# Performance work log

Hardware: AMD Instinct MI355X
Metric: run time of the kernel (lower is better)

The kernel has to match this reference:

```python
import jax, jax.numpy as jnp
import numpy as np

B, T, I, H = 64, 2048, 256, 256


def setup_inputs() -> dict:
    key = jax.random.key(0)
    ks = jax.random.split(key, 9)
    s = 1.0 / np.sqrt(H).astype(np.float32)  # torch nn.RNN init: U(-1/sqrt(H), 1/sqrt(H))
    u = lambda k, shape: jax.random.uniform(k, shape, jnp.float32, -s, s)
    return {
        "input_feature": jax.random.normal(ks[0], (B, T, I), jnp.float32),
        "W_ih0": u(ks[1], (H, I)),
        "W_hh0": u(ks[2], (H, H)),
        "b_ih0": u(ks[3], (H,)),
        "b_hh0": u(ks[4], (H,)),
        "W_ih1": u(ks[5], (H, H)),
        "W_hh1": u(ks[6], (H, H)),
        "b_ih1": u(ks[7], (H,)),
        "b_hh1": u(ks[8], (H,)),
    }


def _rnn_layer(x, W_ih, W_hh, b_ih, b_hh):
    # x: [B, T, F]. Precompute the input projection for all timesteps at once,
    # then scan the recurrence: h_t = tanh(x_t W_ih^T + b_ih + h_{t-1} W_hh^T + b_hh)
    pre = jnp.einsum("btf,hf->bth", x, W_ih) + b_ih + b_hh  # [B, T, H]
    h0 = jnp.zeros((x.shape[0], W_hh.shape[0]), x.dtype)

    def step(h, p):
        h_new = jnp.tanh(p + h @ W_hh.T)
        return h_new, h_new

    _, ys = jax.lax.scan(step, h0, jnp.swapaxes(pre, 0, 1))  # [T, B, H]
    return jnp.swapaxes(ys, 0, 1)  # [B, T, H]


def reference(input_feature, W_ih0, W_hh0, b_ih0, b_hh0, W_ih1, W_hh1, b_ih1, b_hh1):
    # hidden_0 = zeros, batch_first=True, tanh nonlinearity (torch.nn.RNN default)
    h = _rnn_layer(input_feature, W_ih0, W_hh0, b_ih0, b_hh0)
    h = _rnn_layer(h, W_ih1, W_hh1, b_ih1, b_hh1)
    return h  # output: [B, T, H] (module returns only `output`)
```

## Files before the change

kernel.cpp:

```cpp
#include <hip/hip_runtime.h>
#include <stdint.h>

#define B_ 64
#define T_ 2048
#define H_ 256
#define S_ 64
#define C_ (T_ / S_)

typedef unsigned int u32;
typedef unsigned short u16;
typedef __attribute__((ext_vector_type(8))) short short8;
typedef __attribute__((ext_vector_type(4))) float f32x4;

#define SWZ(row, byte) (((row) * 512) + ((byte) ^ (((row) & 7) << 4)))

static __device__ __forceinline__ u32 cvtpk(float a, float b) {
  u32 d;
  asm("v_cvt_pk_bf16_f32 %0, %1, %2" : "=v"(d) : "v"(a), "v"(b));
  return d;
}
static __device__ __forceinline__ uint4 pack8(float4 a, float4 b) {
  uint4 r;
  r.x = cvtpk(a.x, a.y); r.y = cvtpk(a.z, a.w);
  r.z = cvtpk(b.x, b.y); r.w = cvtpk(b.z, b.w);
  return r;
}
static __device__ __forceinline__ short8 as8(uint4 v) {
  return __builtin_bit_cast(short8, v);
}
static __device__ __forceinline__ f32x4 mfma4(uint4 a, uint4 b, f32x4 c) {
  return __builtin_amdgcn_mfma_f32_16x16x32_bf16(as8(a), as8(b), c, 0, 0, 0);
}
static __device__ __forceinline__ float fast_tanh(float x) {
  float e = __expf(2.0f * x);
  float r = __builtin_amdgcn_rcpf(e + 1.0f);
  return fmaf(-2.0f, r, 1.0f);
}

template <int NQ>
static __device__ __forceinline__ void load_wfrag(const float* W, int qbase, int bl,
                                                  int g, uint4 wf[NQ][8]) {
#pragma unroll
  for (int q = 0; q < NQ; ++q) {
    const float* wr = W + (size_t)((qbase + q) * 16 + bl) * H_ + g * 8;
#pragma unroll
    for (int kc = 0; kc < 8; ++kc) {
      float4 a = *(const float4*)(wr + kc * 32);
      float4 b = *(const float4*)(wr + kc * 32 + 4);
      wf[q][kc] = pack8(a, b);
    }
  }
}

static __device__ void proj0_body(char* smem, const float* X, const float* Wih0,
                                  const float* bih0, const float* bhh0,
                                  float* dout, int ch, int bid2) {
  const int tid = threadIdx.x;
  const int lane = tid & 63, wv = tid >> 6;
  const int bl = lane & 15, g = lane >> 4;
  char* sb0 = smem;
  char* sb1 = smem + 8192;

  uint4 wf[2][8];
  load_wfrag<2>(Wih0, wv * 2, bl, g, wf);
  float4 cb[2];
#pragma unroll
  for (int q = 0; q < 2; ++q) {
    const int j0 = (wv * 2 + q) * 16 + g * 4;
    float4 a = *(const float4*)(bih0 + j0);
    float4 b = *(const float4*)(bhh0 + j0);
    cb[q].x = a.x + b.x; cb[q].y = a.y + b.y;
    cb[q].z = a.z + b.z; cb[q].w = a.w + b.w;
  }

  const int sr = tid >> 5, sc8 = (tid & 31) * 8;
  auto rowbase = [&](int it) -> size_t {
    const int b = bid2 * 2 + (it >> 2), i = it & 3;
    return (size_t)(b * T_ + ch * S_ + i * 16);
  };
  float4 s0, s1;
  {
    const float4* xs = (const float4*)(X + (rowbase(0) + sr) * H_ + sc8);
    s0 = xs[0]; s1 = xs[1];
  }

  for (int it = 0; it < 8; ++it) {
    char* sb = (it & 1) ? sb1 : sb0;
    *(uint4*)(sb + SWZ(sr, sc8 * 2)) = pack8(s0, s1);
    __syncthreads();
    if (it + 1 < 8) {
      const float4* xn = (const float4*)(X + (rowbase(it + 1) + sr) * H_ + sc8);
      s0 = xn[0]; s1 = xn[1];
    }
    uint4 hf[8];
#pragma unroll
    for (int kc = 0; kc < 8; ++kc)
      hf[kc] = *(const uint4*)(sb + SWZ(bl, kc * 64 + g * 16));
    f32x4 acc[2];
#pragma unroll
    for (int q = 0; q < 2; ++q) {
      acc[q] = (f32x4){0.f, 0.f, 0.f, 0.f};
#pragma unroll
      for (int kc = 0; kc < 8; ++kc)
        acc[q] = mfma4(wf[q][kc], hf[kc], acc[q]);
    }
    float* od = dout + (rowbase(it) + bl) * H_;
#pragma unroll
    for (int q = 0; q < 2; ++q) {
      const int j0 = (wv * 2 + q) * 16 + g * 4;
      float4 o;
      o.x = acc[q][0] + cb[q].x; o.y = acc[q][1] + cb[q].y;
      o.z = acc[q][2] + cb[q].z; o.w = acc[q][3] + cb[q].w;
      *(float4*)(od + j0) = o;
    }
    __syncthreads();
  }
}

__global__ __launch_bounds__(512, 1) void pre_chunk0(const float* X, const float* Wih0,
                                                     const float* bih0, const float* bhh0,
                                                     float* dout) {
  __shared__ __align__(16) char smem[2 * 8192];
  proj0_body(smem, X, Wih0, bih0, bhh0, dout, 0, blockIdx.x);
}

__global__ __launch_bounds__(256, 2) void pre_mfma(const float* X, const float* W,
                                                   const float* bi, const float* bh,
                                                   float* P, int tpw) {
  __shared__ char sb_[2][8192];
  const int tid = threadIdx.x;
  const int lane = tid & 63, wv = tid >> 6;
  const int bl = lane & 15, g = lane >> 4;

  uint4 wf[4][8];
  load_wfrag<4>(W, wv * 4, bl, g, wf);
  float4 bias[4];
#pragma unroll
  for (int q = 0; q < 4; ++q) {
    const int j0 = (wv * 4 + q) * 16 + g * 4;
    float4 a = *(const float4*)(bi + j0);
    float4 c = *(const float4*)(bh + j0);
    bias[q].x = a.x + c.x; bias[q].y = a.y + c.y;
    bias[q].z = a.z + c.z; bias[q].w = a.w + c.w;
  }

  const size_t row0 = (size_t)blockIdx.x * tpw * 16;
  const int sr = tid >> 4, sc = (tid & 15) * 16;
  float4 s0, s1, s2, s3;
  {
    const float4* xs = (const float4*)(X + (row0 + sr) * H_ + sc);
    s0 = xs[0]; s1 = xs[1]; s2 = xs[2]; s3 = xs[3];
  }

  for (int i = 0; i < tpw; ++i) {
    char* sb = sb_[i & 1];
    *(uint4*)(sb + SWZ(sr, sc * 2)) = pack8(s0, s1);
    *(uint4*)(sb + SWZ(sr, sc * 2 + 16)) = pack8(s2, s3);
    __syncthreads();
    if (i + 1 < tpw) {
      const float4* xn = (const float4*)(X + (row0 + (i + 1) * 16 + sr) * H_ + sc);
      s0 = xn[0]; s1 = xn[1]; s2 = xn[2]; s3 = xn[3];
    }
    uint4 hf[8];
#pragma unroll
    for (int kc = 0; kc < 8; ++kc)
      hf[kc] = *(const uint4*)(sb + SWZ(bl, kc * 64 + g * 16));
    f32x4 acc[4];
#pragma unroll
    for (int q = 0; q < 4; ++q) {
      acc[q] = (f32x4){0.f, 0.f, 0.f, 0.f};
#pragma unroll
      for (int kc = 0; kc < 8; ++kc)
        acc[q] = mfma4(wf[q][kc], hf[kc], acc[q]);
    }
#pragma unroll
    for (int q = 0; q < 4; ++q) {
      const int j0 = (wv * 4 + q) * 16 + g * 4;
      float4 o;
      o.x = acc[q][0] + bias[q].x; o.y = acc[q][1] + bias[q].y;
      o.z = acc[q][2] + bias[q].z; o.w = acc[q][3] + bias[q].w;
      *(float4*)(P + (row0 + i * 16 + bl) * H_ + j0) = o;
    }
    __syncthreads();
  }
}

__global__ __launch_bounds__(512, 1) void rec_mfma(const float* pre, const float* W,
                                                   float* out) {
  __shared__ char hb_[2][8192];
  const int tid = threadIdx.x;
  const int lane = tid & 63, wv = tid >> 6;
  const int bl = lane & 15, g = lane >> 4;
  const int b0 = blockIdx.x * 16;

  uint4 wf[2][8];
  load_wfrag<2>(W, wv * 2, bl, g, wf);
  {
    uint4 z = make_uint4(0, 0, 0, 0);
    ((uint4*)hb_[0])[tid] = z;
    ((uint4*)hb_[1])[tid] = z;
  }
  const float* prow = pre + (size_t)(b0 + bl) * T_ * H_;
  float* orow = out + (size_t)(b0 + bl) * T_ * H_;
  float4 pr0[2], pr1[2];
#pragma unroll
  for (int q = 0; q < 2; ++q) {
    const int j0 = (wv * 2 + q) * 16 + g * 4;
    pr0[q] = *(const float4*)(prow + 0 * H_ + j0);
    pr1[q] = *(const float4*)(prow + 1 * H_ + j0);
  }
  __syncthreads();

  auto step = [&](int t, float4 (&pr)[2], char* rbuf, char* wbuf) {
    uint4 hf[8];
#pragma unroll
    for (int kc = 0; kc < 8; ++kc)
      hf[kc] = *(const uint4*)(rbuf + SWZ(bl, kc * 64 + g * 16));
    f32x4 accA[2], accB[2];
#pragma unroll
    for (int q = 0; q < 2; ++q) {
      accA[q] = (f32x4){0.f, 0.f, 0.f, 0.f};
      accB[q] = (f32x4){0.f, 0.f, 0.f, 0.f};
#pragma unroll
      for (int kc = 0; kc < 4; ++kc) {
        accA[q] = mfma4(wf[q][kc], hf[kc], accA[q]);
        accB[q] = mfma4(wf[q][kc + 4], hf[kc + 4], accB[q]);
      }
    }
#pragma unroll
    for (int q = 0; q < 2; ++q) {
      const int j0 = (wv * 2 + q) * 16 + g * 4;
      const float* pq = (const float*)&pr[q];
      float v0 = fast_tanh(accA[q][0] + accB[q][0] + pq[0]);
      float v1 = fast_tanh(accA[q][1] + accB[q][1] + pq[1]);
      float v2 = fast_tanh(accA[q][2] + accB[q][2] + pq[2]);
      float v3 = fast_tanh(accA[q][3] + accB[q][3] + pq[3]);
      uint2 hw; hw.x = cvtpk(v0, v1); hw.y = cvtpk(v2, v3);
      *(uint2*)(wbuf + SWZ(bl, j0 * 2)) = hw;
      float4 o; o.x = v0; o.y = v1; o.z = v2; o.w = v3;
      *(float4*)(orow + (size_t)t * H_ + j0) = o;
      if (t + 2 < T_)
        pr[q] = *(const float4*)(prow + (size_t)(t + 2) * H_ + j0);
    }
    asm volatile("s_waitcnt lgkmcnt(0)" ::: "memory");
    __builtin_amdgcn_s_barrier();
    __builtin_amdgcn_sched_barrier(0);
  };

  for (int t = 0; t < T_; t += 2) {
    step(t, pr0, hb_[0], hb_[1]);
    step(t + 1, pr1, hb_[1], hb_[0]);
  }
}

__global__ __launch_bounds__(512, 1) void chunk4_k(
    const float* X, float* dout, const float* Wih0, const float* bih0,
    const float* bhh0, const float* Whh0, const float* Wih1, const float* Whh1,
    const float* bih1, const float* bhh1,
    u16* ring, u16* carry0, u16* carry1, int c) {
  __shared__ __align__(16) char smem[2 * 8192];
  const int tid = threadIdx.x;
  const int lane = tid & 63, wv = tid >> 6;
  const int bl = lane & 15, g = lane >> 4;
  const int bid = blockIdx.x;
  char* sb0 = smem;
  char* sb1 = smem + 8192;

  if (bid < 4) {
    if (c >= C_) return;
    const int pair = bid;
    uint4 wf[2][8];
    load_wfrag<2>(Whh0, wv * 2, bl, g, wf);
    if (c == 0) {
      uint4 z = make_uint4(0, 0, 0, 0);
      ((uint4*)sb0)[tid] = z;
    } else {
      const u16* cr = carry0 + pair * 16 * H_ + bl * H_;
#pragma unroll
      for (int q = 0; q < 2; ++q) {
        const int j0 = (wv * 2 + q) * 16 + g * 4;
        uint2 hw = *(const uint2*)(cr + j0);
        *(uint2*)(sb0 + SWZ(bl, j0 * 2)) = hw;
      }
    }
    const float* prow = dout + (size_t)(pair * 16 + bl) * T_ * H_ + (size_t)c * S_ * H_;
    u16* rch = ring + ((size_t)(c & 1) * S_) * (B_ * H_) + (size_t)(pair * 16 + bl) * H_;
    float4 pr0[2], pr1[2];
#pragma unroll
    for (int q = 0; q < 2; ++q) {
      const int j0 = (wv * 2 + q) * 16 + g * 4;
      pr0[q] = *(const float4*)(prow + 0 * H_ + j0);
      pr1[q] = *(const float4*)(prow + 1 * H_ + j0);
    }
    __syncthreads();

    auto step = [&](int s, float4 (&pr)[2], char* rbuf, char* wbuf) {
      uint4 hf[8];
#pragma unroll
      for (int kc = 0; kc < 8; ++kc)
        hf[kc] = *(const uint4*)(rbuf + SWZ(bl, kc * 64 + g * 16));
      f32x4 accA[2], accB[2];
#pragma unroll
      for (int q = 0; q < 2; ++q) {
        accA[q] = (f32x4){0.f, 0.f, 0.f, 0.f};
        accB[q] = (f32x4){0.f, 0.f, 0.f, 0.f};
#pragma unroll
        for (int kc = 0; kc < 4; ++kc) {
          accA[q] = mfma4(wf[q][kc], hf[kc], accA[q]);
          accB[q] = mfma4(wf[q][kc + 4], hf[kc + 4], accB[q]);
        }
      }
#pragma unroll
      for (int q = 0; q < 2; ++q) {
        const int j0 = (wv * 2 + q) * 16 + g * 4;
        const float* pq = (const float*)&pr[q];
        float v0 = fast_tanh(accA[q][0] + accB[q][0] + pq[0]);
        float v1 = fast_tanh(accA[q][1] + accB[q][1] + pq[1]);
        float v2 = fast_tanh(accA[q][2] + accB[q][2] + pq[2]);
        float v3 = fast_tanh(accA[q][3] + accB[q][3] + pq[3]);
        uint2 hw; hw.x = cvtpk(v0, v1); hw.y = cvtpk(v2, v3);
        *(uint2*)(wbuf + SWZ(bl, j0 * 2)) = hw;
        *(uint2*)(rch + (size_t)s * (B_ * H_) + j0) = hw;
        if (s + 2 < S_)
          pr[q] = *(const float4*)(prow + (size_t)(s + 2) * H_ + j0);
      }
      asm volatile("s_waitcnt lgkmcnt(0)" ::: "memory");
      __builtin_amdgcn_s_barrier();
      __builtin_amdgcn_sched_barrier(0);
    };
    for (int s = 0; s < S_; s += 2) {
      step(s, pr0, sb0, sb1);
      step(s + 1, pr1, sb1, sb0);
    }
    {
      u16* cw = carry0 + pair * 16 * H_ + bl * H_;
#pragma unroll
      for (int q = 0; q < 2; ++q) {
        const int j0 = (wv * 2 + q) * 16 + g * 4;
        uint2 hw = *(const uint2*)(sb0 + SWZ(bl, j0 * 2));
        *(uint2*)(cw + j0) = hw;
      }
    }
  } else if (bid < 8) {
    if (c < 1 || c > C_) return;
    const int pair = bid - 4;
    const int ch = c - 1;
    uint4 wf[2][8];
    load_wfrag<2>(Wih1, wv * 2, bl, g, wf);
    float4 cb[2];
#pragma unroll
    for (int q = 0; q < 2; ++q) {
      const int j0 = (wv * 2 + q) * 16 + g * 4;
      float4 a = *(const float4*)(bih1 + j0);
      float4 b = *(const float4*)(bhh1 + j0);
      cb[q].x = a.x + b.x; cb[q].y = a.y + b.y;
      cb[q].z = a.z + b.z; cb[q].w = a.w + b.w;
    }
    const u16* rbase2 = ring + ((size_t)(ch & 1) * S_) * (B_ * H_) + (size_t)pair * 16 * H_;
    const int sr = tid >> 5, scb = (tid & 31) * 16;
    uint4 v = *(const uint4*)(rbase2 + 0 * (B_ * H_) + (size_t)sr * H_ + (tid & 31) * 8);

    for (int s = 0; s < S_; ++s) {
      char* sb = (s & 1) ? sb1 : sb0;
      *(uint4*)(sb + SWZ(sr, scb)) = v;
      __syncthreads();
      if (s + 1 < S_)
        v = *(const uint4*)(rbase2 + (size_t)(s + 1) * (B_ * H_) + (size_t)sr * H_ + (tid & 31) * 8);
      uint4 hf[8];
#pragma unroll
      for (int kc = 0; kc < 8; ++kc)
        hf[kc] = *(const uint4*)(sb + SWZ(bl, kc * 64 + g * 16));
      f32x4 acc[2];
#pragma unroll
      for (int q = 0; q < 2; ++q) {
        acc[q] = (f32x4){0.f, 0.f, 0.f, 0.f};
#pragma unroll
        for (int kc = 0; kc < 8; ++kc)
          acc[q] = mfma4(wf[q][kc], hf[kc], acc[q]);
      }
      float* od = dout + (size_t)(pair * 16 + bl) * T_ * H_ + (size_t)(ch * S_ + s) * H_;
#pragma unroll
      for (int q = 0; q < 2; ++q) {
        const int j0 = (wv * 2 + q) * 16 + g * 4;
        float4 o;
        o.x = acc[q][0] + cb[q].x; o.y = acc[q][1] + cb[q].y;
        o.z = acc[q][2] + cb[q].z; o.w = acc[q][3] + cb[q].w;
        *(float4*)(od + j0) = o;
      }
      __syncthreads();
    }
  } else if (bid < 12) {
    if (c < 2) return;
    const int pair = bid - 8;
    const int ch = c - 2;
    uint4 wf[2][8];
    load_wfrag<2>(Whh1, wv * 2, bl, g, wf);
    if (ch == 0) {
      uint4 z = make_uint4(0, 0, 0, 0);
      ((uint4*)sb0)[tid] = z;
    } else {
      const u16* cr = carry1 + pair * 16 * H_ + bl * H_;
#pragma unroll
      for (int q = 0; q < 2; ++q) {
        const int j0 = (wv * 2 + q) * 16 + g * 4;
        uint2 hw = *(const uint2*)(cr + j0);
        *(uint2*)(sb0 + SWZ(bl, j0 * 2)) = hw;
      }
    }
    float* prow = dout + (size_t)(pair * 16 + bl) * T_ * H_ + (size_t)ch * S_ * H_;
    float4 pr0[2], pr1[2];
#pragma unroll
    for (int q = 0; q < 2; ++q) {
      const int j0 = (wv * 2 + q) * 16 + g * 4;
      pr0[q] = *(const float4*)(prow + 0 * H_ + j0);
      pr1[q] = *(const float4*)(prow + 1 * H_ + j0);
    }
    __syncthreads();

    auto step = [&](int s, float4 (&pr)[2], char* rbuf, char* wbuf) {
      uint4 hf[8];
#pragma unroll
      for (int kc = 0; kc < 8; ++kc)
        hf[kc] = *(const uint4*)(rbuf + SWZ(bl, kc * 64 + g * 16));
      f32x4 accA[2], accB[2];
#pragma unroll
      for (int q = 0; q < 2; ++q) {
        accA[q] = (f32x4){0.f, 0.f, 0.f, 0.f};
        accB[q] = (f32x4){0.f, 0.f, 0.f, 0.f};
#pragma unroll
        for (int kc = 0; kc < 4; ++kc) {
          accA[q] = mfma4(wf[q][kc], hf[kc], accA[q]);
          accB[q] = mfma4(wf[q][kc + 4], hf[kc + 4], accB[q]);
        }
      }
#pragma unroll
      for (int q = 0; q < 2; ++q) {
        const int j0 = (wv * 2 + q) * 16 + g * 4;
        const float* pq = (const float*)&pr[q];
        float v0 = fast_tanh(accA[q][0] + accB[q][0] + pq[0]);
        float v1 = fast_tanh(accA[q][1] + accB[q][1] + pq[1]);
        float v2 = fast_tanh(accA[q][2] + accB[q][2] + pq[2]);
        float v3 = fast_tanh(accA[q][3] + accB[q][3] + pq[3]);
        uint2 hw; hw.x = cvtpk(v0, v1); hw.y = cvtpk(v2, v3);
        *(uint2*)(wbuf + SWZ(bl, j0 * 2)) = hw;
        float4 o; o.x = v0; o.y = v1; o.z = v2; o.w = v3;
        *(float4*)(prow + (size_t)s * H_ + j0) = o;
        if (s + 2 < S_)
          pr[q] = *(const float4*)(prow + (size_t)(s + 2) * H_ + j0);
      }
      asm volatile("s_waitcnt lgkmcnt(0)" ::: "memory");
      __builtin_amdgcn_s_barrier();
      __builtin_amdgcn_sched_barrier(0);
    };
    for (int s = 0; s < S_; s += 2) {
      step(s, pr0, sb0, sb1);
      step(s + 1, pr1, sb1, sb0);
    }
    {
      u16* cw = carry1 + pair * 16 * H_ + bl * H_;
#pragma unroll
      for (int q = 0; q < 2; ++q) {
        const int j0 = (wv * 2 + q) * 16 + g * 4;
        uint2 hw = *(const uint2*)(sb0 + SWZ(bl, j0 * 2));
        *(uint2*)(cw + j0) = hw;
      }
    }
  } else {
    if (c + 1 > C_ - 1) return;
    proj0_body(smem, X, Wih0, bih0, bhh0, dout, c + 1, bid - 12);
  }
}

extern "C" void kernel_launch(void* const* d_in, const int* in_sizes, int n_in,
                              void* d_out, int out_size, void* d_ws, size_t ws_size,
                              hipStream_t stream) {
  (void)in_sizes; (void)n_in; (void)out_size;
  const float* x    = (const float*)d_in[0];
  const float* Wih0 = (const float*)d_in[1];
  const float* Whh0 = (const float*)d_in[2];
  const float* bih0 = (const float*)d_in[3];
  const float* bhh0 = (const float*)d_in[4];
  const float* Wih1 = (const float*)d_in[5];
  const float* Whh1 = (const float*)d_in[6];
  const float* bih1 = (const float*)d_in[7];
  const float* bhh1 = (const float*)d_in[8];
  float* out = (float*)d_out;

  const size_t ring_elems = (size_t)2 * S_ * B_ * H_;
  const size_t carry_elems = (size_t)B_ * H_;
  const size_t need = (ring_elems + 2 * carry_elems) * sizeof(u16);

  if (ws_size >= need) {
    u16* ring = (u16*)d_ws;
    u16* carry0 = ring + ring_elems;
    u16* carry1 = carry0 + carry_elems;
    pre_chunk0<<<dim3(32), dim3(512), 0, stream>>>(x, Wih0, bih0, bhh0, out);
    for (int c = 0; c <= C_ + 1; ++c)
      chunk4_k<<<dim3(44), dim3(512), 0, stream>>>(
          x, out, Wih0, bih0, bhh0, Whh0, Wih1, Whh1, bih1, bhh1,
          ring, carry0, carry1, c);
  } else {
    const int TPW = 8;
    const int NWG = (B_ * T_) / (TPW * 16);
    pre_mfma<<<dim3(NWG), dim3(256), 0, stream>>>(x, Wih0, bih0, bhh0, out, TPW);
    rec_mfma<<<dim3(B_ / 16), dim3(512), 0, stream>>>(out, Whh0, out);
    pre_mfma<<<dim3(NWG), dim3(256), 0, stream>>>(out, Wih1, bih1, bhh1, out, TPW);
    rec_mfma<<<dim3(B_ / 16), dim3(512), 0, stream>>>(out, Whh1, out);
  }
}
```

Before: 2.431 ms.

## Replace per-chunk kernel launches with one persistent kernel using flag-based sync

```diff
diff --git a/kernel.cpp b/kernel.cpp
--- a/kernel.cpp
+++ b/kernel.cpp
@@ -52,26 +52,37 @@
   }
 }
 
+static __device__ __forceinline__ void wait_ge(u32* f, u32 tgt) {
+  if (__hip_atomic_load(f, __ATOMIC_ACQUIRE, __HIP_MEMORY_SCOPE_AGENT) >= tgt) return;
+  while (__hip_atomic_load(f, __ATOMIC_ACQUIRE, __HIP_MEMORY_SCOPE_AGENT) < tgt)
+    __builtin_amdgcn_s_sleep(8);
+}
+static __device__ __forceinline__ void drain_all() {
+  asm volatile("s_waitcnt vmcnt(0) lgkmcnt(0)" ::: "memory");
+  __builtin_amdgcn_s_barrier();
+}
+static __device__ __forceinline__ void publish_val(u32* f, u32 v) {
+  drain_all();
+  if (threadIdx.x == 0)
+    __hip_atomic_store(f, v, __ATOMIC_RELEASE, __HIP_MEMORY_SCOPE_AGENT);
+}
+static __device__ __forceinline__ void publish_add(u32* f) {
+  drain_all();
+  if (threadIdx.x == 0)
+    (void)__hip_atomic_fetch_add(f, 1u, __ATOMIC_RELEASE, __HIP_MEMORY_SCOPE_AGENT);
+}
+
+__global__ void init_flags(u32* f) { f[threadIdx.x] = 0; }
+
 static __device__ void proj0_body(char* smem, const float* X, const float* Wih0,
                                   const float* bih0, const float* bhh0,
-                                  float* dout, int ch, int bid2) {
+                                  float* dout, int ch, int bid2,
+                                  const uint4 wf[2][8], const float4 cb[2]) {
   const int tid = threadIdx.x;
   const int lane = tid & 63, wv = tid >> 6;
   const int bl = lane & 15, g = lane >> 4;
   char* sb0 = smem;
   char* sb1 = smem + 8192;
-
-  uint4 wf[2][8];
-  load_wfrag<2>(Wih0, wv * 2, bl, g, wf);
-  float4 cb[2];
-#pragma unroll
-  for (int q = 0; q < 2; ++q) {
-    const int j0 = (wv * 2 + q) * 16 + g * 4;
-    float4 a = *(const float4*)(bih0 + j0);
-    float4 b = *(const float4*)(bhh0 + j0);
-    cb[q].x = a.x + b.x; cb[q].y = a.y + b.y;
-    cb[q].z = a.z + b.z; cb[q].w = a.w + b.w;
-  }
 
   const int sr = tid >> 5, sc8 = (tid & 31) * 8;
   auto rowbase = [&](int it) -> size_t {
@@ -83,7 +94,6 @@
     const float4* xs = (const float4*)(X + (rowbase(0) + sr) * H_ + sc8);
     s0 = xs[0]; s1 = xs[1];
   }
-
   for (int it = 0; it < 8; ++it) {
     char* sb = (it & 1) ? sb1 : sb0;
     *(uint4*)(sb + SWZ(sr, sc8 * 2)) = pack8(s0, s1);
@@ -115,13 +125,6 @@
     }
     __syncthreads();
   }
-}
-
-__global__ __launch_bounds__(512, 1) void pre_chunk0(const float* X, const float* Wih0,
-                                                     const float* bih0, const float* bhh0,
-                                                     float* dout) {
-  __shared__ __align__(16) char smem[2 * 8192];
-  proj0_body(smem, X, Wih0, bih0, bhh0, dout, 0, blockIdx.x);
 }
 
 __global__ __launch_bounds__(256, 2) void pre_mfma(const float* X, const float* W,
@@ -143,7 +146,6 @@
     bias[q].x = a.x + c.x; bias[q].y = a.y + c.y;
     bias[q].z = a.z + c.z; bias[q].w = a.w + c.w;
   }
-
   const size_t row0 = (size_t)blockIdx.x * tpw * 16;
   const int sr = tid >> 4, sc = (tid & 15) * 16;
   float4 s0, s1, s2, s3;
@@ -151,7 +153,6 @@
     const float4* xs = (const float4*)(X + (row0 + sr) * H_ + sc);
     s0 = xs[0]; s1 = xs[1]; s2 = xs[2]; s3 = xs[3];
   }
-
   for (int i = 0; i < tpw; ++i) {
     char* sb = sb_[i & 1];
     *(uint4*)(sb + SWZ(sr, sc * 2)) = pack8(s0, s1);
@@ -246,18 +247,17 @@
     __builtin_amdgcn_s_barrier();
     __builtin_amdgcn_sched_barrier(0);
   };
-
   for (int t = 0; t < T_; t += 2) {
     step(t, pr0, hb_[0], hb_[1]);
     step(t + 1, pr1, hb_[1], hb_[0]);
   }
 }
 
-__global__ __launch_bounds__(512, 1) void chunk4_k(
-    const float* X, float* dout, const float* Wih0, const float* bih0,
-    const float* bhh0, const float* Whh0, const float* Wih1, const float* Whh1,
-    const float* bih1, const float* bhh1,
-    u16* ring, u16* carry0, u16* carry1, int c) {
+__global__ __launch_bounds__(512, 1) void persist_k(
+    const float* X, float* dout,
+    const float* Wih0, const float* bih0, const float* bhh0, const float* Whh0,
+    const float* Wih1, const float* Whh1, const float* bih1, const float* bhh1,
+    u16* ring, u32* flags) {
   __shared__ __align__(16) char smem[2 * 8192];
   const int tid = threadIdx.x;
   const int lane = tid & 63, wv = tid >> 6;
@@ -265,86 +265,74 @@
   const int bid = blockIdx.x;
   char* sb0 = smem;
   char* sb1 = smem + 8192;
+  u32* proj0_cnt = flags;
+  auto rec0_prog = [&](int p) { return flags + 32 + 32 * p; };
+  auto proj1_prog = [&](int p) { return flags + 160 + 32 * p; };
 
   if (bid < 4) {
-    if (c >= C_) return;
-    const int pair = bid;
+    const int p = bid;
     uint4 wf[2][8];
     load_wfrag<2>(Whh0, wv * 2, bl, g, wf);
-    if (c == 0) {
-      uint4 z = make_uint4(0, 0, 0, 0);
-      ((uint4*)sb0)[tid] = z;
-    } else {
-      const u16* cr = carry0 + pair * 16 * H_ + bl * H_;
+    { uint4 z = make_uint4(0, 0, 0, 0); ((uint4*)sb0)[tid] = z; }
+    __syncthreads();
+    const float* prow = dout + (size_t)(p * 16 + bl) * T_ * H_;
+    u16* rb = ring + (size_t)(p * 16 + bl) * H_;
+
+    for (int c = 0; c < C_; ++c) {
+      const u32 ptgt = 32u * (u32)((c + 2 < C_) ? (c + 2) : C_);
+      wait_ge(proj0_cnt, ptgt);
+      if (c >= 1) wait_ge(proj1_prog(p), (u32)(c - 1));
+      const float* pch = prow + (size_t)c * S_ * H_;
+      u16* rch = rb + ((size_t)(c & 1) * S_) * (B_ * H_);
+      float4 pr0[2], pr1[2];
 #pragma unroll
       for (int q = 0; q < 2; ++q) {
         const int j0 = (wv * 2 + q) * 16 + g * 4;
-        uint2 hw = *(const uint2*)(cr + j0);
-        *(uint2*)(sb0 + SWZ(bl, j0 * 2)) = hw;
-      }
-    }
-    const float* prow = dout + (size_t)(pair * 16 + bl) * T_ * H_ + (size_t)c * S_ * H_;
-    u16* rch = ring + ((size_t)(c & 1) * S_) * (B_ * H_) + (size_t)(pair * 16 + bl) * H_;
-    float4 pr0[2], pr1[2];
-#pragma unroll
-    for (int q = 0; q < 2; ++q) {
-      const int j0 = (wv * 2 + q) * 16 + g * 4;
-      pr0[q] = *(const float4*)(prow + 0 * H_ + j0);
-      pr1[q] = *(const float4*)(prow + 1 * H_ + j0);
-    }
-    __syncthreads();
-
-    auto step = [&](int s, float4 (&pr)[2], char* rbuf, char* wbuf) {
-      uint4 hf[8];
-#pragma unroll
-      for (int kc = 0; kc < 8; ++kc)
-        hf[kc] = *(const uint4*)(rbuf + SWZ(bl, kc * 64 + g * 16));
-      f32x4 accA[2], accB[2];
-#pragma unroll
-      for (int q = 0; q < 2; ++q) {
-        accA[q] = (f32x4){0.f, 0.f, 0.f, 0.f};
-        accB[q] = (f32x4){0.f, 0.f, 0.f, 0.f};
-#pragma unroll
-        for (int kc = 0; kc < 4; ++kc) {
-          accA[q] = mfma4(wf[q][kc], hf[kc], accA[q]);
-          accB[q] = mfma4(wf[q][kc + 4], hf[kc + 4], accB[q]);
-        }
-      }
-#pragma unroll
-      for (int q = 0; q < 2; ++q) {
-        const int j0 = (wv * 2 + q) * 16 + g * 4;
-        const float* pq = (const float*)&pr[q];
-        float v0 = fast_tanh(accA[q][0] + accB[q][0] + pq[0]);
-        float v1 = fast_tanh(accA[q][1] + accB[q][1] + pq[1]);
-        float v2 = fast_tanh(accA[q][2] + accB[q][2] + pq[2]);
-        float v3 = fast_tanh(accA[q][3] + accB[q][3] + pq[3]);
-        uint2 hw; hw.x = cvtpk(v0, v1); hw.y = cvtpk(v2, v3);
-        *(uint2*)(wbuf + SWZ(bl, j0 * 2)) = hw;
-        *(uint2*)(rch + (size_t)s * (B_ * H_) + j0) = hw;
-        if (s + 2 < S_)
-          pr[q] = *(const float4*)(prow + (size_t)(s + 2) * H_ + j0);
-      }
-      asm volatile("s_waitcnt lgkmcnt(0)" ::: "memory");
-      __builtin_amdgcn_s_barrier();
-      __builtin_amdgcn_sched_barrier(0);
-    };
-    for (int s = 0; s < S_; s += 2) {
-      step(s, pr0, sb0, sb1);
-      step(s + 1, pr1, sb1, sb0);
-    }
-    {
-      u16* cw = carry0 + pair * 16 * H_ + bl * H_;
-#pragma unroll
-      for (int q = 0; q < 2; ++q) {
-        const int j0 = (wv * 2 + q) * 16 + g * 4;
-        uint2 hw = *(const uint2*)(sb0 + SWZ(bl, j0 * 2));
-        *(uint2*)(cw + j0) = hw;
-      }
+        pr0[q] = *(const float4*)(pch + 0 * H_ + j0);
+        pr1[q] = *(const float4*)(pch + 1 * H_ + j0);
+      }
+      auto step = [&](int s, float4 (&pr)[2], char* rbuf, char* wbuf) {
+        uint4 hf[8];
+#pragma unroll
+        for (int kc = 0; kc < 8; ++kc)
+          hf[kc] = *(const uint4*)(rbuf + SWZ(bl, kc * 64 + g * 16));
+        f32x4 accA[2], accB[2];
+#pragma unroll
+        for (int q = 0; q < 2; ++q) {
+          accA[q] = (f32x4){0.f, 0.f, 0.f, 0.f};
+          accB[q] = (f32x4){0.f, 0.f, 0.f, 0.f};
+#pragma unroll
+          for (int kc = 0; kc < 4; ++kc) {
+            accA[q] = mfma4(wf[q][kc], hf[kc], accA[q]);
+            accB[q] = mfma4(wf[q][kc + 4], hf[kc + 4], accB[q]);
+          }
+        }
+#pragma unroll
+        for (int q = 0; q < 2; ++q) {
+          const int j0 = (wv * 2 + q) * 16 + g * 4;
+          const float* pq = (const float*)&pr[q];
+          float v0 = fast_tanh(accA[q][0] + accB[q][0] + pq[0]);
+          float v1 = fast_tanh(accA[q][1] + accB[q][1] + pq[1]);
+          float v2 = fast_tanh(accA[q][2] + accB[q][2] + pq[2]);
+          float v3 = fast_tanh(accA[q][3] + accB[q][3] + pq[3]);
+          uint2 hw; hw.x = cvtpk(v0, v1); hw.y = cvtpk(v2, v3);
+          *(uint2*)(wbuf + SWZ(bl, j0 * 2)) = hw;
+          *(uint2*)(rch + (size_t)s * (B_ * H_) + j0) = hw;
+          if (s + 2 < S_)
+            pr[q] = *(const float4*)(pch + (size_t)(s + 2) * H_ + j0);
+        }
+        asm volatile("s_waitcnt lgkmcnt(0)" ::: "memory");
+        __builtin_amdgcn_s_barrier();
+        __builtin_amdgcn_sched_barrier(0);
+      };
+      for (int s = 0; s < S_; s += 2) {
+        step(s, pr0, sb0, sb1);
+        step(s + 1, pr1, sb1, sb0);
+      }
+      publish_val(rec0_prog(p), (u32)(c + 1));
     }
   } else if (bid < 8) {
-    if (c < 1 || c > C_) return;
-    const int pair = bid - 4;
-    const int ch = c - 1;
+    const int p = bid - 4;
     uint4 wf[2][8];
     load_wfrag<2>(Wih1, wv * 2, bl, g, wf);
     float4 cb[2];
@@ -356,118 +344,117 @@
       cb[q].x = a.x + b.x; cb[q].y = a.y + b.y;
       cb[q].z = a.z + b.z; cb[q].w = a.w + b.w;
     }
-    const u16* rbase2 = ring + ((size_t)(ch & 1) * S_) * (B_ * H_) + (size_t)pair * 16 * H_;
     const int sr = tid >> 5, scb = (tid & 31) * 16;
-    uint4 v = *(const uint4*)(rbase2 + 0 * (B_ * H_) + (size_t)sr * H_ + (tid & 31) * 8);
-
-    for (int s = 0; s < S_; ++s) {
-      char* sb = (s & 1) ? sb1 : sb0;
-      *(uint4*)(sb + SWZ(sr, scb)) = v;
-      __syncthreads();
-      if (s + 1 < S_)
-        v = *(const uint4*)(rbase2 + (size_t)(s + 1) * (B_ * H_) + (size_t)sr * H_ + (tid & 31) * 8);
-      uint4 hf[8];
-#pragma unroll
-      for (int kc = 0; kc < 8; ++kc)
-        hf[kc] = *(const uint4*)(sb + SWZ(bl, kc * 64 + g * 16));
-      f32x4 acc[2];
-#pragma unroll
-      for (int q = 0; q < 2; ++q) {
-        acc[q] = (f32x4){0.f, 0.f, 0.f, 0.f};
+    for (int ch = 0; ch < C_; ++ch) {
+      wait_ge(rec0_prog(p), (u32)(ch + 1));
+      const u16* rbase2 = ring + ((size_t)(ch & 1) * S_) * (B_ * H_) + (size_t)p * 16 * H_;
+      uint4 v = *(const uint4*)(rbase2 + (size_t)sr * H_ + (tid & 31) * 8);
+      for (int s = 0; s < S_; ++s) {
+        char* sb = (s & 1) ? sb1 : sb0;
+        *(uint4*)(sb + SWZ(sr, scb)) = v;
+        __syncthreads();
+        if (s + 1 < S_)
+          v = *(const uint4*)(rbase2 + (size_t)(s + 1) * (B_ * H_) + (size_t)sr * H_ + (tid & 31) * 8);
+        uint4 hf[8];
 #pragma unroll
         for (int kc = 0; kc < 8; ++kc)
-          acc[q] = mfma4(wf[q][kc], hf[kc], acc[q]);
-      }
-      float* od = dout + (size_t)(pair * 16 + bl) * T_ * H_ + (size_t)(ch * S_ + s) * H_;
+          hf[kc] = *(const uint4*)(sb + SWZ(bl, kc * 64 + g * 16));
+        f32x4 acc[2];
+#pragma unroll
+        for (int q = 0; q < 2; ++q) {
+          acc[q] = (f32x4){0.f, 0.f, 0.f, 0.f};
+#pragma unroll
+          for (int kc = 0; kc < 8; ++kc)
+            acc[q] = mfma4(wf[q][kc], hf[kc], acc[q]);
+        }
+        float* od = dout + (size_t)(p * 16 + bl) * T_ * H_ + (size_t)(ch * S_ + s) * H_;
+#pragma unroll
+        for (int q = 0; q < 2; ++q) {
+          const int j0 = (wv * 2 + q) * 16 + g * 4;
+          float4 o;
+          o.x = acc[q][0] + cb[q].x; o.y = acc[q][1] + cb[q].y;
+          o.z = acc[q][2] + cb[q].z; o.w = acc[q][3] + cb[q].w;
+          *(float4*)(od + j0) = o;
+        }
+        __syncthreads();
+      }
+      publish_val(proj1_prog(p), (u32)(ch + 1));
+    }
+  } else if (bid < 12) {
+    const int p = bid - 8;
+    uint4 wf[2][8];
+    load_wfrag<2>(Whh1, wv * 2, bl, g, wf);
+    { uint4 z = make_uint4(0, 0, 0, 0); ((uint4*)sb0)[tid] = z; }
+    __syncthreads();
+    float* prow = dout + (size_t)(p * 16 + bl) * T_ * H_;
+
+    for (int ch = 0; ch < C_; ++ch) {
+      wait_ge(proj1_prog(p), (u32)(ch + 1));
+      float* pch = prow + (size_t)ch * S_ * H_;
+      float4 pr0[2], pr1[2];
 #pragma unroll
       for (int q = 0; q < 2; ++q) {
         const int j0 = (wv * 2 + q) * 16 + g * 4;
-        float4 o;
-        o.x = acc[q][0] + cb[q].x; o.y = acc[q][1] + cb[q].y;
-        o.z = acc[q][2] + cb[q].z; o.w = acc[q][3] + cb[q].w;
-        *(float4*)(od + j0) = o;
-      }
-      __syncthreads();
-    }
-  } else if (bid < 12) {
-    if (c < 2) return;
-    const int pair = bid - 8;
-    const int ch = c - 2;
+        pr0[q] = *(const float4*)(pch + 0 * H_ + j0);
+        pr1[q] = *(const float4*)(pch + 1 * H_ + j0);
+      }
+      auto step = [&](int s, float4 (&pr)[2], char* rbuf, char* wbuf) {
+        uint4 hf[8];
+#pragma unroll
+        for (int kc = 0; kc < 8; ++kc)
+          hf[kc] = *(const uint4*)(rbuf + SWZ(bl, kc * 64 + g * 16));
+        f32x4 accA[2], accB[2];
+#pragma unroll
+        for (int q = 0; q < 2; ++q) {
+          accA[q] = (f32x4){0.f, 0.f, 0.f, 0.f};
+          accB[q] = (f32x4){0.f, 0.f, 0.f, 0.f};
+#pragma unroll
+          for (int kc = 0; kc < 4; ++kc) {
+            accA[q] = mfma4(wf[q][kc], hf[kc], accA[q]);
+            accB[q] = mfma4(wf[q][kc + 4], hf[kc + 4], accB[q]);
+          }
+        }
+#pragma unroll
+        for (int q = 0; q < 2; ++q) {
+          const int j0 = (wv * 2 + q) * 16 + g * 4;
+          const float* pq = (const float*)&pr[q];
+          float v0 = fast_tanh(accA[q][0] + accB[q][0] + pq[0]);
+          float v1 = fast_tanh(accA[q][1] + accB[q][1] + pq[1]);
+          float v2 = fast_tanh(accA[q][2] + accB[q][2] + pq[2]);
+          float v3 = fast_tanh(accA[q][3] + accB[q][3] + pq[3]);
+          uint2 hw; hw.x = cvtpk(v0, v1); hw.y = cvtpk(v2, v3);
+          *(uint2*)(wbuf + SWZ(bl, j0 * 2)) = hw;
+          float4 o; o.x = v0; o.y = v1; o.z = v2; o.w = v3;
+          *(float4*)(pch + (size_t)s * H_ + j0) = o;
+          if (s + 2 < S_)
+            pr[q] = *(const float4*)(pch + (size_t)(s + 2) * H_ + j0);
+        }
+        asm volatile("s_waitcnt lgkmcnt(0)" ::: "memory");
+        __builtin_amdgcn_s_barrier();
+        __builtin_amdgcn_sched_barrier(0);
+      };
+      for (int s = 0; s < S_; s += 2) {
+        step(s, pr0, sb0, sb1);
+        step(s + 1, pr1, sb1, sb0);
+      }
+    }
+  } else {
+    const int b2 = bid - 12;
     uint4 wf[2][8];
-    load_wfrag<2>(Whh1, wv * 2, bl, g, wf);
-    if (ch == 0) {
-      uint4 z = make_uint4(0, 0, 0, 0);
-      ((uint4*)sb0)[tid] = z;
-    } else {
-      const u16* cr = carry1 + pair * 16 * H_ + bl * H_;
-#pragma unroll
-      for (int q = 0; q < 2; ++q) {
-        const int j0 = (wv * 2 + q) * 16 + g * 4;
-        uint2 hw = *(const uint2*)(cr + j0);
-        *(uint2*)(sb0 + SWZ(bl, j0 * 2)) = hw;
-      }
-    }
-    float* prow = dout + (size_t)(pair * 16 + bl) * T_ * H_ + (size_t)ch * S_ * H_;
-    float4 pr0[2], pr1[2];
+    load_wfrag<2>(Wih0, wv * 2, bl, g, wf);
+    float4 cb[2];
 #pragma unroll
     for (int q = 0; q < 2; ++q) {
       const int j0 = (wv * 2 + q) * 16 + g * 4;
-      pr0[q] = *(const float4*)(prow + 0 * H_ + j0);
-      pr1[q] = *(const float4*)(prow + 1 * H_ + j0);
-    }
-    __syncthreads();
-
-    auto step = [&](int s, float4 (&pr)[2], char* rbuf, char* wbuf) {
-      uint4 hf[8];
-#pragma unroll
-      for (int kc = 0; kc < 8; ++kc)
-        hf[kc] = *(const uint4*)(rbuf + SWZ(bl, kc * 64 + g * 16));
-      f32x4 accA[2], accB[2];
-#pragma unroll
-      for (int q = 0; q < 2; ++q) {
-        accA[q] = (f32x4){0.f, 0.f, 0.f, 0.f};
-        accB[q] = (f32x4){0.f, 0.f, 0.f, 0.f};
-#pragma unroll
-        for (int kc = 0; kc < 4; ++kc) {
-          accA[q] = mfma4(wf[q][kc], hf[kc], accA[q]);
-          accB[q] = mfma4(wf[q][kc + 4], hf[kc + 4], accB[q]);
-        }
-      }
-#pragma unroll
-      for (int q = 0; q < 2; ++q) {
-        const int j0 = (wv * 2 + q) * 16 + g * 4;
-        const float* pq = (const float*)&pr[q];
-        float v0 = fast_tanh(accA[q][0] + accB[q][0] + pq[0]);
-        float v1 = fast_tanh(accA[q][1] + accB[q][1] + pq[1]);
-        float v2 = fast_tanh(accA[q][2] + accB[q][2] + pq[2]);
-        float v3 = fast_tanh(accA[q][3] + accB[q][3] + pq[3]);
-        uint2 hw; hw.x = cvtpk(v0, v1); hw.y = cvtpk(v2, v3);
-        *(uint2*)(wbuf + SWZ(bl, j0 * 2)) = hw;
-        float4 o; o.x = v0; o.y = v1; o.z = v2; o.w = v3;
-        *(float4*)(prow + (size_t)s * H_ + j0) = o;
-        if (s + 2 < S_)
-          pr[q] = *(const float4*)(prow + (size_t)(s + 2) * H_ + j0);
-      }
-      asm volatile("s_waitcnt lgkmcnt(0)" ::: "memory");
-      __builtin_amdgcn_s_barrier();
-      __builtin_amdgcn_sched_barrier(0);
-    };
-    for (int s = 0; s < S_; s += 2) {
-      step(s, pr0, sb0, sb1);
-      step(s + 1, pr1, sb1, sb0);
-    }
-    {
-      u16* cw = carry1 + pair * 16 * H_ + bl * H_;
-#pragma unroll
-      for (int q = 0; q < 2; ++q) {
-        const int j0 = (wv * 2 + q) * 16 + g * 4;
-        uint2 hw = *(const uint2*)(sb0 + SWZ(bl, j0 * 2));
-        *(uint2*)(cw + j0) = hw;
-      }
-    }
-  } else {
-    if (c + 1 > C_ - 1) return;
-    proj0_body(smem, X, Wih0, bih0, bhh0, dout, c + 1, bid - 12);
+      float4 a = *(const float4*)(bih0 + j0);
+      float4 b = *(const float4*)(bhh0 + j0);
+      cb[q].x = a.x + b.x; cb[q].y = a.y + b.y;
+      cb[q].z = a.z + b.z; cb[q].w = a.w + b.w;
+    }
+    for (int c = 0; c < C_; ++c) {
+      proj0_body(smem, X, Wih0, bih0, bhh0, dout, c, b2, wf, cb);
+      publish_add(proj0_cnt);
+    }
   }
 }
 
@@ -486,19 +473,15 @@
   const float* bhh1 = (const float*)d_in[8];
   float* out = (float*)d_out;
 
-  const size_t ring_elems = (size_t)2 * S_ * B_ * H_;
-  const size_t carry_elems = (size_t)B_ * H_;
-  const size_t need = (ring_elems + 2 * carry_elems) * sizeof(u16);
+  const size_t ring_bytes = (size_t)2 * S_ * B_ * H_ * sizeof(u16);
+  const size_t need = 4096 + ring_bytes;
 
   if (ws_size >= need) {
-    u16* ring = (u16*)d_ws;
-    u16* carry0 = ring + ring_elems;
-    u16* carry1 = carry0 + carry_elems;
-    pre_chunk0<<<dim3(32), dim3(512), 0, stream>>>(x, Wih0, bih0, bhh0, out);
-    for (int c = 0; c <= C_ + 1; ++c)
-      chunk4_k<<<dim3(44), dim3(512), 0, stream>>>(
-          x, out, Wih0, bih0, bhh0, Whh0, Wih1, Whh1, bih1, bhh1,
-          ring, carry0, carry1, c);
+    u32* flags = (u32*)d_ws;
+    u16* ring = (u16*)((char*)d_ws + 4096);
+    init_flags<<<dim3(1), dim3(1024), 0, stream>>>(flags);
+    persist_k<<<dim3(44), dim3(512), 0, stream>>>(
+        x, out, Wih0, bih0, bhh0, Whh0, Wih1, Whh1, bih1, bhh1, ring, flags);
   } else {
     const int TPW = 8;
     const int NWG = (B_ * T_) / (TPW * 16);
```

New measurement: 2.154 ms. 1.13x faster.
